# Kernel optimization log

Measured on AMD Instinct MI355X. Metric: run time of the kernel, lower is better.

The kernel has to match this reference:

```python
import jax, jax.numpy as jnp
import numpy as np

B, C_ENC, H, W = 8, 512, 96, 96
N_SAMP = 64            # num_samples in forward
N_NODES = 2 * N_SAMP   # 64 pos + 64 neg per image
D = 256                # node feature dim after head_in_ln
N_HEADS = 8
DH = D // N_HEADS
SINKHORN_ITERS = 10


def _ln(x):
    # LayerNorm(elementwise_affine=False)
    m = x.mean(-1, keepdims=True)
    v = x.var(-1, keepdims=True)
    return (x - m) / jnp.sqrt(v + 1e-5)


def setup_inputs() -> dict:
    key = jax.random.key(0)
    ks = jax.random.split(key, 12)
    std = 0.01  # matches nn.init.normal_(std=0.01) in _init_weights
    inp = {
        "feat_s": jax.random.normal(ks[0], (B, C_ENC, H, W), jnp.float32),
        "score_s": jax.random.normal(ks[1], (B, 1, H, W), jnp.float32),
        "feat_t": jax.random.normal(ks[2], (B, C_ENC, H, W), jnp.float32),
        "score_t": jax.random.normal(ks[3], (B, 1, H, W), jnp.float32),
        "head_W1": std * jax.random.normal(ks[4], (C_ENC, D), jnp.float32),
        "head_b1": jnp.zeros((D,), jnp.float32),
        "head_W2": std * jax.random.normal(ks[5], (D, D), jnp.float32),
        "head_b2": jnp.zeros((D,), jnp.float32),
        "intra_W": jax.random.normal(ks[6], (4, D, D), jnp.float32) / jnp.sqrt(jnp.float32(D)),
        "intra_b": jnp.zeros((4, D), jnp.float32),
        "cross_W": jax.random.normal(ks[7], (4, D, D), jnp.float32) / jnp.sqrt(jnp.float32(D)),
        "cross_b": jnp.zeros((4, D), jnp.float32),
        "cls_W1": std * jax.random.normal(ks[8], (D, 128), jnp.float32),
        "cls_b1": jnp.zeros((128,), jnp.float32),
        "cls_W2": std * jax.random.normal(ks[9], (128, 1), jnp.float32),
        "cls_b2": jnp.zeros((1,), jnp.float32),
        "aff_A": jax.random.normal(ks[10], (D, D), jnp.float32) / jnp.sqrt(jnp.float32(D)),
    }
    return inp


def _sample_points(feat, score):
    # torch version: boolean-mask nonzero + random gather of 64 pos / 64 neg spatial
    # locations per image. JIT-friendly deterministic equivalent: top-64 highest
    # sigmoid scores = positives, top-64 lowest = negatives.
    s = jax.nn.sigmoid(score[:, 0].reshape(B, -1))            # [B, H*W]
    _, pos_idx = jax.lax.top_k(s, N_SAMP)
    _, neg_idx = jax.lax.top_k(-s, N_SAMP)
    idx = jnp.concatenate([pos_idx, neg_idx], axis=1)         # [B, 128]
    ff = feat.reshape(B, C_ENC, -1)                           # [B, 512, H*W]
    nodes = jnp.take_along_axis(ff, idx[:, None, :], axis=2)  # [B, 512, 128]
    nodes = nodes.transpose(0, 2, 1)                          # [B, 128, 512]
    labels = jnp.concatenate(
        [jnp.ones((B, N_SAMP, 1), feat.dtype), jnp.zeros((B, N_SAMP, 1), feat.dtype)], axis=1)
    return nodes, labels


def _mha(xq, xkv, Wp, bp):
    # standard multi-head attention (MultiHeadAttentionWrapper)
    q = xq @ Wp[0] + bp[0]
    k = xkv @ Wp[1] + bp[1]
    v = xkv @ Wp[2] + bp[2]
    sh = lambda t: t.reshape(t.shape[0], t.shape[1], N_HEADS, DH)
    att = jnp.einsum("bqhd,bkhd->bhqk", sh(q), sh(k)) / jnp.sqrt(jnp.float32(DH))
    att = jax.nn.softmax(att, axis=-1)
    o = jnp.einsum("bhqk,bkhd->bqhd", att, sh(v)).reshape(xq.shape[0], xq.shape[1], D)
    return o @ Wp[3] + bp[3], att.mean(1)


def _forward(feat_s, score_s, feat_t, score_t, head_W1, head_b1, head_W2, head_b2,
             intra_W, intra_b, cross_W, cross_b, cls_W1, cls_b1, cls_W2, cls_b2, aff_A):
    n1, l1 = _sample_points(feat_s, score_s)
    n2, l2 = _sample_points(feat_t, score_t)

    # head_in_ln: Linear -> LN -> ReLU -> Linear -> LN
    head = lambda x: _ln(jax.nn.relu(_ln(x @ head_W1 + head_b1)) @ head_W2 + head_b2)
    n1, n2 = head(n1), head(n2)

    # intra-domain graph (self-attention), shared weights for both domains
    n1, _ = _mha(n1, n1, intra_W, intra_b)
    n2, _ = _mha(n2, n2, intra_W, intra_b)

    # cross-domain graph (cross-attention both directions, shared weights)
    c1, _ = _mha(n1, n2, cross_W, cross_b)
    c2, _ = _mha(n2, n1, cross_W, cross_b)
    n1, n2 = c1, c2

    # node classification loss (BCEWithLogits, mean)
    cls = lambda x: jax.nn.relu(x @ cls_W1 + cls_b1) @ cls_W2 + cls_b2
    def bce_logits(logit, lab):
        return jnp.mean(jnp.maximum(logit, 0) - logit * lab + jnp.log1p(jnp.exp(-jnp.abs(logit))))
    node_loss = bce_logits(cls(n1), l1) + bce_logits(cls(n2), l2)

    # affinity + InstanceNorm2d(1) + sinkhorn refine
    Mmat = jnp.einsum("bnd,de,bme->bnm", n1, aff_A, n2)       # [B, 128, 128]
    mu = Mmat.mean((1, 2), keepdims=True)
    var = Mmat.var((1, 2), keepdims=True)
    K = (Mmat - mu) / jnp.sqrt(var + 1e-5)
    for _ in range(SINKHORN_ITERS):  # log-space row/col normalization
        K = K - jax.nn.logsumexp(K, axis=2, keepdims=True)
        K = K - jax.nn.logsumexp(K, axis=1, keepdims=True)
    P = jnp.exp(K)

    # matching loss = BCEFocalLoss(gamma=2, alpha=0.25) vs label-agreement matrix
    gt = (l1[:, :, 0][:, :, None] == l2[:, :, 0][:, None, :]).astype(P.dtype)
    pt = jnp.clip(P, 1e-6, 1.0 - 1e-6)
    mat_loss = jnp.mean(-0.25 * (1 - pt) ** 2 * gt * jnp.log(pt)
                        - 0.75 * pt ** 2 * (1 - gt) * jnp.log(1 - pt))

    total_loss = node_loss + 10.0 * mat_loss
    return n1, total_loss


def reference(feat_s, score_s, feat_t, score_t, head_W1, head_b1, head_W2, head_b2,
              intra_W, intra_b, cross_W, cross_b, cls_W1, cls_b1, cls_W2, cls_b2, aff_A):
    return _forward(feat_s, score_s, feat_t, score_t, head_W1, head_b1, head_W2, head_b2,
                    intra_W, intra_b, cross_W, cross_b, cls_W1, cls_b1, cls_W2, cls_b2, aff_A)
```

## Files before the change

### kernel.cpp

```cpp
#include <hip/hip_runtime.h>
#include <math.h>

#define BIMG 8
#define HW 9216
#define CENC 512
#define NN 128
#define DD 256
#define NHEAD 8
#define DH 32
#define ROWS1 1024
#define ROWS2 2048
#define TAILB 520

typedef unsigned long long ull;
typedef unsigned short u16;
typedef __attribute__((ext_vector_type(4))) float f32x4;
typedef __attribute__((ext_vector_type(4))) unsigned u32x4;
typedef __attribute__((ext_vector_type(2))) unsigned u32x2;

__device__ __forceinline__ u16 f2bf(float f) {
  unsigned u = __float_as_uint(f);
  u += 0x7fffu + ((u >> 16) & 1u);
  return (u16)(u >> 16);
}
__device__ __forceinline__ float bf2f(unsigned h) { return __uint_as_float(h << 16); }
__device__ __forceinline__ unsigned pack2(float a, float b) {
  return (unsigned)f2bf(a) | ((unsigned)f2bf(b) << 16);
}
__device__ __forceinline__ void mfma_b(f32x4& acc, u32x4 a, u32x4 b) {
  asm volatile("v_mfma_f32_16x16x32_bf16 %0, %1, %2, %0" : "+v"(acc) : "v"(a), "v"(b));
}

__device__ __forceinline__ ull cmpex_keep(ull k, ull o, bool keepMax) {
  return ((k > o) == keepMax) ? k : o;
}
__device__ __forceinline__ void bsort64(ull& k, int lane) {
#pragma unroll
  for (int size = 2; size <= 64; size <<= 1) {
#pragma unroll
    for (int stride = size >> 1; stride > 0; stride >>= 1) {
      ull o = __shfl_xor(k, stride);
      bool keepMax = (((lane & size) == 0) == ((lane & stride) == 0));
      k = cmpex_keep(k, o, keepMax);
    }
  }
}
__device__ __forceinline__ void bmerge64(ull& top, ull b, int lane) {
  ull rev = __shfl_xor(b, 63);
  ull m = top > rev ? top : rev;
#pragma unroll
  for (int stride = 32; stride > 0; stride >>= 1) {
    ull o = __shfl_xor(m, stride);
    m = cmpex_keep(m, o, (lane & stride) == 0);
  }
  top = m;
}

__global__ __launch_bounds__(256) void head_kernel(const float* __restrict__ score_s,
                                                   const float* __restrict__ score_t,
                                                   int* __restrict__ idx_out,
                                                   float* __restrict__ loss_acc,
                                                   const float* __restrict__ hw1,
                                                   const float* __restrict__ hw2,
                                                   const float* __restrict__ iw,
                                                   const float* __restrict__ cw,
                                                   const float* __restrict__ aw,
                                                   const float* __restrict__ clsW1,
                                                   u16* __restrict__ wt,
                                                   u16* __restrict__ w1t) {
  __shared__ ull sm[256];
  __shared__ float tile[32][33];
  int tid = threadIdx.x;
  if (blockIdx.x < 32) {
    int blk = blockIdx.x;
    int bi = blk >> 1, neg = blk & 1;
    int lane = tid & 63, w = tid >> 6;
    if (blk == 0 && tid < 4) loss_acc[tid] = 0.f;
    const float* sp = (bi < 8 ? score_s : score_t) + (size_t)(bi & 7) * HW;
    int q0 = w * 36;
    ull keys[36];
#pragma unroll
    for (int j = 0; j < 36; ++j) {
      float x = sp[(q0 + j) * 64 + lane];
      unsigned ub = __float_as_uint(x);
      unsigned u = (ub & 0x80000000u) ? ~ub : (ub | 0x80000000u);
      if (neg) u = ~u;
      int gi = (q0 + j) * 64 + lane;
      keys[j] = ((ull)u << 32) | (unsigned)(~gi);
    }
    ull top1 = keys[0];  bsort64(top1, lane);
    ull top2 = keys[18]; bsort64(top2, lane);
#pragma unroll
    for (int j = 1; j < 18; ++j) {
      ull k1 = keys[j], k2 = keys[18 + j];
      bsort64(k1, lane);
      bsort64(k2, lane);
      bmerge64(top1, k1, lane);
      bmerge64(top2, k2, lane);
    }
    bmerge64(top1, top2, lane);
    sm[w * 64 + lane] = top1;
    __syncthreads();
    if (w < 2) {
      ull a = sm[(2 * w) * 64 + lane];
      ull b = sm[(2 * w + 1) * 64 + (63 - lane)];
      ull m = a > b ? a : b;
#pragma unroll
      for (int stride = 32; stride > 0; stride >>= 1) {
        ull o = __shfl_xor(m, stride);
        m = cmpex_keep(m, o, (lane & stride) == 0);
      }
      sm[(2 * w) * 64 + lane] = m;
    }
    __syncthreads();
    if (w == 0) {
      ull a = sm[lane];
      ull b = sm[128 + (63 - lane)];
      ull m = a > b ? a : b;
#pragma unroll
      for (int stride = 32; stride > 0; stride >>= 1) {
        ull o = __shfl_xor(m, stride);
        m = cmpex_keep(m, o, (lane & stride) == 0);
      }
      idx_out[bi * NN + neg * 64 + lane] = (int)(~(unsigned)(m & 0xffffffffull));
    }
  } else if (blockIdx.x < 800) {
    int bid = blockIdx.x - 32;
    const float* src; u16* dst; int K, k0, n0;
    if (bid < 128) {
      src = hw1; dst = wt; K = 512;
      k0 = (bid >> 3) * 32; n0 = (bid & 7) * 32;
    } else {
      int id2 = bid - 128;
      int m = id2 >> 6, tt = id2 & 63;
      K = 256;
      k0 = (tt >> 3) * 32; n0 = (tt & 7) * 32;
      src = (m == 0) ? hw2 : (m < 5) ? iw + (size_t)(m - 1) * 65536
          : (m < 9) ? cw + (size_t)(m - 5) * 65536 : aw;
      dst = wt + 131072 + (size_t)m * 65536;
    }
    int r = tid >> 3, c = (tid & 7) * 4;
    float4 v = *(const float4*)&src[(size_t)(k0 + r) * 256 + n0 + c];
    tile[r][c] = v.x; tile[r][c + 1] = v.y; tile[r][c + 2] = v.z; tile[r][c + 3] = v.w;
    __syncthreads();
    u32x2 o;
    o[0] = pack2(tile[c][r], tile[c + 1][r]);
    o[1] = pack2(tile[c + 2][r], tile[c + 3][r]);
    *(u32x2*)&dst[(size_t)(n0 + r) * K + k0 + c] = o;
  } else {
    int bid3 = blockIdx.x - 800;
    int k0 = (bid3 >> 2) * 32, n0 = (bid3 & 3) * 32;
    int r = tid >> 3, c = (tid & 7) * 4;
    float4 v = *(const float4*)&clsW1[(size_t)(k0 + r) * 128 + n0 + c];
    tile[r][c] = v.x; tile[r][c + 1] = v.y; tile[r][c + 2] = v.z; tile[r][c + 3] = v.w;
    __syncthreads();
    u32x2 o;
    o[0] = pack2(tile[c][r], tile[c + 1][r]);
    o[1] = pack2(tile[c + 2][r], tile[c + 3][r]);
    *(u32x2*)&w1t[(size_t)(n0 + r) * 256 + k0 + c] = o;
  }
}

__global__ __launch_bounds__(256) void gemm1_fused(const float* __restrict__ feat_s,
                                                   const float* __restrict__ feat_t,
                                                   const int* __restrict__ idxb,
                                                   const u16* __restrict__ wt_h1,
                                                   const float* __restrict__ head_b1,
                                                   u16* __restrict__ bufA,
                                                   float* __restrict__ st1) {
  __shared__ u16 As[16][520];
  __shared__ u16 Bs[256][40];
  int t = threadIdx.x, l = t & 63, cg = t >> 6;
  int m0 = blockIdx.x * 16;
#pragma unroll
  for (int row = 0; row < 16; ++row) {
    int grow = m0 + row;
    int bi = grow >> 7, n = grow & 127, b = bi & 7;
    const float* fp = (bi < 8) ? feat_s : feat_t;
    int pos = idxb[bi * NN + n];
    const float* src = fp + (size_t)b * CENC * HW + pos;
    float f0 = src[(size_t)(2 * t) * HW];
    float f1 = src[(size_t)(2 * t + 1) * HW];
    *(unsigned*)&As[row][2 * t] = pack2(f0, f1);
  }
  __syncthreads();
  f32x4 acc[4];
#pragma unroll
  for (int i = 0; i < 4; ++i) acc[i] = (f32x4){0.f, 0.f, 0.f, 0.f};
  for (int kc = 0; kc < 16; ++kc) {
#pragma unroll
    for (int i = 0; i < 4; ++i) {
      int e = t + i * 256;
      int nn2 = e >> 2, ch8 = (e & 3) * 8;
      *(u32x4*)&Bs[nn2][ch8] = *(const u32x4*)&wt_h1[(size_t)nn2 * 512 + kc * 32 + ch8];
    }
    __syncthreads();
    u32x4 af = *(const u32x4*)&As[l & 15][kc * 32 + (l >> 4) * 8];
#pragma unroll
    for (int i = 0; i < 4; ++i) {
      u32x4 bf = *(const u32x4*)&Bs[cg * 64 + i * 16 + (l & 15)][(l >> 4) * 8];
      mfma_b(acc[i], af, bf);
    }
    __syncthreads();
  }
  asm volatile("s_nop 7\n\ts_nop 7" ::);
  int rbase = m0 + (l >> 4) * 4;
#pragma unroll
  for (int i = 0; i < 4; ++i) {
    int col = cg * 64 + i * 16 + (l & 15);
    float bb = head_b1[col];
#pragma unroll
    for (int r = 0; r < 4; ++r) {
      int row = rbase + r;
      float o = acc[i][r] + bb;
      bufA[(size_t)row * 256 + col] = f2bf(o);
      float s = o, q = o * o;
#pragma unroll
      for (int m = 1; m < 16; m <<= 1) { s += __shfl_xor(s, m); q += __shfl_xor(q, m); }
      if ((l & 15) == 0) {
        st1[(size_t)row * 32 + cg * 4 + i]      = s;
        st1[(size_t)row * 32 + 16 + cg * 4 + i] = q;
      }
    }
  }
}

template<int K>
__global__ __launch_bounds__(256) void gemm_mf(const u16* __restrict__ A,
                                               const u16* __restrict__ Wt,
                                               const float* __restrict__ bias,
                                               u16* __restrict__ Cb,
                                               float* __restrict__ Cf,
                                               int ldc, int f32rows,
                                               const float* __restrict__ in_stats, int in_relu,
                                               float* __restrict__ out_stats,
                                               int Az, int Wz, int Cbz, int Cfz, int bz) {
  constexpr int LDK = K + 8;
  constexpr int KC = K / 8;
  __shared__ u16 As[32][LDK];
  __shared__ u16 Bs[64][LDK];
  __shared__ float mS[32], rS[32];
  int z = blockIdx.z;
  A  += (size_t)z * Az;
  Wt += (size_t)z * Wz;
  if (Cb)   Cb += (size_t)z * Cbz;
  if (Cf)   Cf += (size_t)z * Cfz;
  if (bias) bias += (size_t)z * bz;
  int n0 = blockIdx.x * 64, m0 = blockIdx.y * 32;
  int t = threadIdx.x;
  if (in_stats) {
    if (t < 32) {
      const float* sp = in_stats + (size_t)(m0 + t) * 32;
      float s = 0.f, q = 0.f;
#pragma unroll
      for (int i = 0; i < 16; ++i) { s += sp[i]; q += sp[16 + i]; }
      float mm = s * (1.f / 256.f);
      float var = q * (1.f / 256.f) - mm * mm;
      mS[t] = mm;
      rS[t] = rsqrtf(fmaxf(var, 0.f) + 1e-5f);
    }
    __syncthreads();
  }
  for (int i = t; i < 32 * KC; i += 256) {
    int row = i / KC, c8 = (i % KC) * 8;
    u32x4 av = *(const u32x4*)&A[(size_t)(m0 + row) * K + c8];
    if (in_stats) {
      float mm = mS[row], rr = rS[row];
#pragma unroll
      for (int j = 0; j < 4; ++j) {
        float f0 = (bf2f(av[j] & 0xffffu) - mm) * rr;
        float f1 = (bf2f(av[j] >> 16) - mm) * rr;
        if (in_relu) { f0 = fmaxf(f0, 0.f); f1 = fmaxf(f1, 0.f); }
        av[j] = pack2(f0, f1);
      }
    }
    *(u32x4*)&As[row][c8] = av;
  }
  for (int i = t; i < 64 * KC; i += 256) {
    int row = i / KC, c8 = (i % KC) * 8;
    *(u32x4*)&Bs[row][c8] = *(const u32x4*)&Wt[(size_t)(n0 + row) * K + c8];
  }
  __syncthreads();
  int l = t & 63, w = t >> 6;
  int wr = w >> 1, wc = w & 1;
  int fra = wr * 16 + (l & 15);
  int frk = (l >> 4) * 8;
  int fb0 = wc * 32 + (l & 15), fb1 = fb0 + 16;
  f32x4 acc0 = {0.f, 0.f, 0.f, 0.f};
  f32x4 acc1 = {0.f, 0.f, 0.f, 0.f};
#pragma unroll
  for (int ks = 0; ks < K / 32; ++ks) {
    u32x4 af = *(const u32x4*)&As[fra][ks * 32 + frk];
    u32x4 b0 = *(const u32x4*)&Bs[fb0][ks * 32 + frk];
    u32x4 b1 = *(const u32x4*)&Bs[fb1][ks * 32 + frk];
    mfma_b(acc0, af, b0);
    mfma_b(acc1, af, b1);
  }
  asm volatile("s_nop 7\n\ts_nop 7" ::);
  int col0 = n0 + wc * 32 + (l & 15);
  int rbase = m0 + wr * 16 + (l >> 4) * 4;
  float b0 = 0.f, b1 = 0.f;
  if (bias) { b0 = bias[col0]; b1 = bias[col0 + 16]; }
#pragma unroll
  for (int r = 0; r < 4; ++r) {
    int row = rbase + r;
    float o0 = acc0[r] + b0;
    float o1 = acc1[r] + b1;
    if (Cb) {
      Cb[(size_t)row * 256 + col0]      = f2bf(o0);
      Cb[(size_t)row * 256 + col0 + 16] = f2bf(o1);
    }
    if (Cf && row < ROWS1) {
      Cf[(size_t)row * ldc + col0]      = o0;
      Cf[(size_t)row * ldc + col0 + 16] = o1;
    }
    if (out_stats) {
      float s0 = o0, q0 = o0 * o0, s1 = o1, q1 = o1 * o1;
#pragma unroll
      for (int m = 1; m < 16; m <<= 1) {
        s0 += __shfl_xor(s0, m); q0 += __shfl_xor(q0, m);
        s1 += __shfl_xor(s1, m); q1 += __shfl_xor(q1, m);
      }
      if ((l & 15) == 0) {
        int base = (n0 >> 4) + wc * 2;
        out_stats[(size_t)row * 32 + base]          = s0;
        out_stats[(size_t)row * 32 + base + 1]      = s1;
        out_stats[(size_t)row * 32 + 16 + base]     = q0;
        out_stats[(size_t)row * 32 + 16 + base + 1] = q1;
      }
    }
  }
}

__global__ __launch_bounds__(256) void attn_kernel(const u16* __restrict__ q,
                                                   const u16* __restrict__ k,
                                                   const u16* __restrict__ v,
                                                   u16* __restrict__ o, int swap) {
  __shared__ __align__(16) float Ks[NN][DH];
  __shared__ __align__(16) float Vs[NN][DH];
  __shared__ __align__(16) float Ex[64][3][34];
  int blk = blockIdx.x;
  int bb = blk >> 4, h = (blk >> 1) & 7, qh = blk & 1;
  int kb = swap ? (bb ^ 8) : bb;
  int t = threadIdx.x;
  int rr = t & 63, part = t >> 6;
  for (int e = t; e < 1024; e += 256) {
    int which = e >> 9;
    int idx2 = e & 511;
    int r = idx2 >> 2, c8 = (idx2 & 3) * 8;
    u32x4 val = *(const u32x4*)&(which ? v : k)[(size_t)(kb * NN + r) * DD + h * DH + c8];
    float* dst = which ? &Vs[r][c8] : &Ks[r][c8];
#pragma unroll
    for (int i = 0; i < 4; ++i) {
      dst[2 * i]     = bf2f(val[i] & 0xffffu);
      dst[2 * i + 1] = bf2f(val[i] >> 16);
    }
  }
  __syncthreads();
  int qrow = bb * NN + qh * 64 + rr;
  float4 q4[8];
  {
    const u16* qp = q + (size_t)qrow * DD + h * DH;
#pragma unroll
    for (int c4 = 0; c4 < 4; ++c4) {
      u32x4 u = *(const u32x4*)&qp[c4 * 8];
      q4[c4 * 2].x = bf2f(u[0] & 0xffffu); q4[c4 * 2].y = bf2f(u[0] >> 16);
      q4[c4 * 2].z = bf2f(u[1] & 0xffffu); q4[c4 * 2].w = bf2f(u[1] >> 16);
      q4[c4 * 2 + 1].x = bf2f(u[2] & 0xffffu); q4[c4 * 2 + 1].y = bf2f(u[2] >> 16);
      q4[c4 * 2 + 1].z = bf2f(u[3] & 0xffffu); q4[c4 * 2 + 1].w = bf2f(u[3] >> 16);
    }
  }
  const float scale = 0.17677669529663687f;
  int j0 = part * 32;
  float mx = -1e30f;
  for (int j = j0; j < j0 + 32; ++j) {
    const float4* kp = (const float4*)Ks[j];
    float s = 0.f;
#pragma unroll
    for (int c4 = 0; c4 < 8; ++c4) {
      float4 kv = kp[c4];
      s += q4[c4].x * kv.x + q4[c4].y * kv.y + q4[c4].z * kv.z + q4[c4].w * kv.w;
    }
    mx = fmaxf(mx, s * scale);
  }
  float acc[DH];
#pragma unroll
  for (int c = 0; c < DH; ++c) acc[c] = 0.f;
  float den = 0.f;
  for (int j = j0; j < j0 + 32; ++j) {
    const float4* kp = (const float4*)Ks[j];
    float s = 0.f;
#pragma unroll
    for (int c4 = 0; c4 < 8; ++c4) {
      float4 kv = kp[c4];
      s += q4[c4].x * kv.x + q4[c4].y * kv.y + q4[c4].z * kv.z + q4[c4].w * kv.w;
    }
    float e = __expf(s * scale - mx);
    den += e;
    const float4* vp = (const float4*)Vs[j];
#pragma unroll
    for (int c4 = 0; c4 < 8; ++c4) {
      float4 vv = vp[c4];
      acc[c4 * 4 + 0] += e * vv.x; acc[c4 * 4 + 1] += e * vv.y;
      acc[c4 * 4 + 2] += e * vv.z; acc[c4 * 4 + 3] += e * vv.w;
    }
  }
  if (part) {
#pragma unroll
    for (int c = 0; c < DH; ++c) Ex[rr][part - 1][c] = acc[c];
    Ex[rr][part - 1][32] = mx;
    Ex[rr][part - 1][33] = den;
  }
  __syncthreads();
  if (part == 0) {
    float M = mx;
#pragma unroll
    for (int p = 0; p < 3; ++p) M = fmaxf(M, Ex[rr][p][32]);
    float f0 = __expf(mx - M);
    float fp[3];
    float dt = den * f0;
#pragma unroll
    for (int p = 0; p < 3; ++p) { fp[p] = __expf(Ex[rr][p][32] - M); dt += Ex[rr][p][33] * fp[p]; }
    float inv = 1.0f / dt;
    unsigned ovu[16];
#pragma unroll
    for (int c = 0; c < 16; ++c) {
      float x0 = acc[2 * c] * f0, x1 = acc[2 * c + 1] * f0;
#pragma unroll
      for (int p = 0; p < 3; ++p) { x0 += Ex[rr][p][2 * c] * fp[p]; x1 += Ex[rr][p][2 * c + 1] * fp[p]; }
      ovu[c] = pack2(x0 * inv, x1 * inv);
    }
    unsigned* op = (unsigned*)(o + (size_t)qrow * DD + h * DH);
#pragma unroll
    for (int i = 0; i < 4; ++i) {
      u32x4 w4;
      w4[0] = ovu[4 * i]; w4[1] = ovu[4 * i + 1]; w4[2] = ovu[4 * i + 2]; w4[3] = ovu[4 * i + 3];
      *(u32x4*)&op[4 * i] = w4;
    }
  }
}

struct SkSmem {
  union { u16 tmpL[128][264]; float Km[128][133]; } u;
  float u_[NN];
  float v_[NN];
  float red[20];
};
struct ClsSmem {
  float xs[4][256];
  float part[4][128];
  float red[8];
};
union TailSmem { SkSmem sk; ClsSmem cls; };

__device__ __forceinline__ void ticket_finalize(float* acc, float* out) {
  __threadfence();
  int tk = atomicAdd((int*)acc + 3, 1);
  if (tk == TAILB - 1) {
    float a0 = atomicAdd(acc + 0, 0.0f);
    float a1 = atomicAdd(acc + 1, 0.0f);
    out[ROWS1 * DD] = a0 + 10.0f * a1;
  }
}

__global__ __launch_bounds__(1024) void tail_kernel(const u16* __restrict__ bufH,
                                                    const u16* __restrict__ wt_af,
                                                    const u16* __restrict__ w1t,
                                                    const float* __restrict__ b1,
                                                    const float* __restrict__ W2,
                                                    const float* __restrict__ b2,
                                                    float* __restrict__ acc,
                                                    float* __restrict__ out) {
  __shared__ TailSmem sm;
  int t = threadIdx.x;
  int bid = blockIdx.x;
  if (bid < 8) {
    int b = bid;
    int l = t & 63, w = t >> 6;
    int tr = w >> 1;
    const u16* c1 = bufH + (size_t)(b * 128) * 256;
    const u16* c2 = bufH + (size_t)(1024 + b * 128) * 256;
    {
      int tcB = (w & 1) * 8;
      f32x4 accA[8];
#pragma unroll
      for (int i = 0; i < 8; ++i) accA[i] = (f32x4){0.f, 0.f, 0.f, 0.f};
      for (int ks = 0; ks < 8; ++ks) {
        int kk = ks * 32 + (l >> 4) * 8;
        u32x4 af = *(const u32x4*)&c1[(size_t)(tr * 16 + (l & 15)) * 256 + kk];
#pragma unroll
        for (int i = 0; i < 8; ++i) {
          u32x4 bf = *(const u32x4*)&wt_af[(size_t)((tcB + i) * 16 + (l & 15)) * 256 + kk];
          mfma_b(accA[i], af, bf);
        }
      }
      asm volatile("s_nop 7\n\ts_nop 7" ::);
      int rb = tr * 16 + (l >> 4) * 4;
#pragma unroll
      for (int i = 0; i < 8; ++i) {
        int col = (tcB + i) * 16 + (l & 15);
#pragma unroll
        for (int r2 = 0; r2 < 4; ++r2)
          sm.sk.u.tmpL[rb + r2][col] = f2bf(accA[i][r2]);
      }
    }
    __syncthreads();
    f32x4 aB[4];
    {
      int tcB = (w & 1) * 4;
#pragma unroll
      for (int i = 0; i < 4; ++i) aB[i] = (f32x4){0.f, 0.f, 0.f, 0.f};
      for (int ks = 0; ks < 8; ++ks) {
        int kk = ks * 32 + (l >> 4) * 8;
        u32x4 af = *(const u32x4*)&sm.sk.u.tmpL[tr * 16 + (l & 15)][kk];
#pragma unroll
        for (int i = 0; i < 4; ++i) {
          u32x4 bf = *(const u32x4*)&c2[(size_t)((tcB + i) * 16 + (l & 15)) * 256 + kk];
          mfma_b(aB[i], af, bf);
        }
      }
      asm volatile("s_nop 7\n\ts_nop 7" ::);
    }
    __syncthreads();
    {
      int tcB = (w & 1) * 4;
      int rb = tr * 16 + (l >> 4) * 4;
#pragma unroll
      for (int i = 0; i < 4; ++i) {
        int col = (tcB + i) * 16 + (l & 15);
#pragma unroll
        for (int r2 = 0; r2 < 4; ++r2)
          sm.sk.u.Km[rb + r2][col] = aB[i][r2];
      }
    }
    __syncthreads();
    int r = t >> 3, cg = t & 7;
    int c = t >> 3, rg = t & 7;
    float kr[16], kc[16];
    {
#pragma unroll
      for (int q4 = 0; q4 < 4; ++q4) {
        float4 f = *(const float4*)&sm.sk.u.Km[r][cg * 16 + q4 * 4];
        kr[q4 * 4 + 0] = f.x; kr[q4 * 4 + 1] = f.y; kr[q4 * 4 + 2] = f.z; kr[q4 * 4 + 3] = f.w;
      }
#pragma unroll
      for (int q = 0; q < 16; ++q)
        kc[q] = sm.sk.u.Km[rg * 16 + q][c];
    }
    float s = 0.f;
#pragma unroll
    for (int q = 0; q < 16; ++q) s += kr[q];
    for (int m = 1; m < 64; m <<= 1) s += __shfl_xor(s, m);
    if ((t & 63) == 0) sm.sk.red[t >> 6] = s;
    __syncthreads();
    if (t == 0) { float tt = 0.f; for (int i = 0; i < 16; ++i) tt += sm.sk.red[i]; sm.sk.red[16] = tt; }
    __syncthreads();
    float mu = sm.sk.red[16] * (1.0f / 16384.f);
    __syncthreads();
    float sq = 0.f;
#pragma unroll
    for (int q = 0; q < 16; ++q) { float d = kr[q] - mu; sq += d * d; }
    for (int m = 1; m < 64; m <<= 1) sq += __shfl_xor(sq, m);
    if ((t & 63) == 0) sm.sk.red[t >> 6] = sq;
    __syncthreads();
    if (t == 0) { float tt = 0.f; for (int i = 0; i < 16; ++i) tt += sm.sk.red[i]; sm.sk.red[17] = tt; }
    __syncthreads();
    float inv = 1.0f / sqrtf(sm.sk.red[17] * (1.0f / 16384.f) + 1e-5f);
#pragma unroll
    for (int q = 0; q < 16; ++q) { kr[q] = (kr[q] - mu) * inv; kc[q] = (kc[q] - mu) * inv; }
    if (t < NN) { sm.sk.u_[t] = 0.f; sm.sk.v_[t] = 0.f; }
    __syncthreads();
    for (int iter = 0; iter < 10; ++iter) {
      float tmp[16];
      {
        const float4* vp = (const float4*)(sm.sk.v_ + cg * 16);
#pragma unroll
        for (int q4 = 0; q4 < 4; ++q4) {
          float4 f = vp[q4];
          tmp[q4 * 4 + 0] = kr[q4 * 4 + 0] - f.x; tmp[q4 * 4 + 1] = kr[q4 * 4 + 1] - f.y;
          tmp[q4 * 4 + 2] = kr[q4 * 4 + 2] - f.z; tmp[q4 * 4 + 3] = kr[q4 * 4 + 3] - f.w;
        }
        float mx = tmp[0];
#pragma unroll
        for (int q = 1; q < 16; ++q) mx = fmaxf(mx, tmp[q]);
        for (int m = 1; m < 8; m <<= 1) mx = fmaxf(mx, __shfl_xor(mx, m));
        float smv = 0.f;
#pragma unroll
        for (int q = 0; q < 16; ++q) smv += __expf(tmp[q] - mx);
        for (int m = 1; m < 8; m <<= 1) smv += __shfl_xor(smv, m);
        if (cg == 0) sm.sk.u_[r] = mx + __logf(smv);
      }
      __syncthreads();
      {
        const float4* up = (const float4*)(sm.sk.u_ + rg * 16);
#pragma unroll
        for (int q4 = 0; q4 < 4; ++q4) {
          float4 f = up[q4];
          tmp[q4 * 4 + 0] = kc[q4 * 4 + 0] - f.x; tmp[q4 * 4 + 1] = kc[q4 * 4 + 1] - f.y;
          tmp[q4 * 4 + 2] = kc[q4 * 4 + 2] - f.z; tmp[q4 * 4 + 3] = kc[q4 * 4 + 3] - f.w;
        }
        float mx = tmp[0];
#pragma unroll
        for (int q = 1; q < 16; ++q) mx = fmaxf(mx, tmp[q]);
        for (int m = 1; m < 8; m <<= 1) mx = fmaxf(mx, __shfl_xor(mx, m));
        float smv = 0.f;
#pragma unroll
        for (int q = 0; q < 16; ++q) smv += __expf(tmp[q] - mx);
        for (int m = 1; m < 8; m <<= 1) smv += __shfl_xor(smv, m);
        if (rg == 0) sm.sk.v_[c] = mx + __logf(smv);
      }
      __syncthreads();
    }
    float ur = sm.sk.u_[r];
    float fsum = 0.f;
    {
      const float4* vp = (const float4*)(sm.sk.v_ + cg * 16);
#pragma unroll
      for (int q4 = 0; q4 < 4; ++q4) {
        float4 f = vp[q4];
        float vv[4] = {f.x, f.y, f.z, f.w};
#pragma unroll
        for (int j = 0; j < 4; ++j) {
          float P = __expf(kr[q4 * 4 + j] - ur - vv[j]);
          float pt = fminf(fmaxf(P, 1e-6f), 1.0f - 1e-6f);
          int col = cg * 16 + q4 * 4 + j;
          bool gt = (r < 64) == (col < 64);
          float wgt = gt ? (-0.25f * (1.f - pt) * (1.f - pt)) : (-0.75f * pt * pt);
          float lg = gt ? __logf(pt) : __logf(1.f - pt);
          fsum += wgt * lg;
        }
      }
    }
    for (int m = 1; m < 64; m <<= 1) fsum += __shfl_xor(fsum, m);
    if ((t & 63) == 0) sm.sk.red[t >> 6] = fsum;
    __syncthreads();
    if (t == 0) {
      float tt = 0.f; for (int i = 0; i < 16; ++i) tt += sm.sk.red[i];
      atomicAdd(acc + 1, tt * (1.0f / 131072.f));
      ticket_finalize(acc, out);
    }
  } else {
    int row0 = (bid - 8) * 4;
    {
      int rr = t >> 8, cc = t & 255;
      sm.cls.xs[rr][cc] = bf2f(bufH[(size_t)(row0 + rr) * 256 + cc]);
    }
    __syncthreads();
    int grp = t >> 8, col = t & 127, kh = (t >> 7) & 1;
    const u16* wp = w1t + (size_t)col * 256 + kh * 128;
    const float* xp = &sm.cls.xs[grp][kh * 128];
    float h = 0.f;
#pragma unroll
    for (int i = 0; i < 16; ++i) {
      u32x4 wv = *(const u32x4*)&wp[i * 8];
      const float* x8 = xp + i * 8;
      h += x8[0] * bf2f(wv[0] & 0xffffu) + x8[1] * bf2f(wv[0] >> 16)
         + x8[2] * bf2f(wv[1] & 0xffffu) + x8[3] * bf2f(wv[1] >> 16)
         + x8[4] * bf2f(wv[2] & 0xffffu) + x8[5] * bf2f(wv[2] >> 16)
         + x8[6] * bf2f(wv[3] & 0xffffu) + x8[7] * bf2f(wv[3] >> 16);
    }
    if (kh == 1) sm.cls.part[grp][col] = h;
    __syncthreads();
    if (kh == 0) {
      float z = h + sm.cls.part[grp][col] + b1[col];
      float p = fmaxf(z, 0.f) * W2[col];
#pragma unroll
      for (int m = 1; m < 64; m <<= 1) p += __shfl_xor(p, m);
      if ((t & 63) == 0) sm.cls.red[grp * 2 + ((t >> 6) & 1)] = p;
    }
    __syncthreads();
    if (t == 0) {
      float total = 0.f;
      float bb2 = b2[0];
#pragma unroll
      for (int g = 0; g < 4; ++g) {
        float z = sm.cls.red[2 * g] + sm.cls.red[2 * g + 1] + bb2;
        float lab = (((row0 + g) & 127) < 64) ? 1.f : 0.f;
        total += fmaxf(z, 0.f) - z * lab + log1pf(__expf(-fabsf(z)));
      }
      atomicAdd(acc, total * (1.0f / 1024.0f));
      ticket_finalize(acc, out);
    }
  }
}

extern "C" void kernel_launch(void* const* d_in, const int* in_sizes, int n_in,
                              void* d_out, int out_size, void* d_ws, size_t ws_size,
                              hipStream_t stream) {
  const float* feat_s  = (const float*)d_in[0];
  const float* score_s = (const float*)d_in[1];
  const float* feat_t  = (const float*)d_in[2];
  const float* score_t = (const float*)d_in[3];
  const float* head_W1 = (const float*)d_in[4];
  const float* head_b1 = (const float*)d_in[5];
  const float* head_W2 = (const float*)d_in[6];
  const float* head_b2 = (const float*)d_in[7];
  const float* intra_W = (const float*)d_in[8];
  const float* intra_b = (const float*)d_in[9];
  const float* cross_W = (const float*)d_in[10];
  const float* cross_b = (const float*)d_in[11];
  const float* cls_W1  = (const float*)d_in[12];
  const float* cls_b1  = (const float*)d_in[13];
  const float* cls_W2  = (const float*)d_in[14];
  const float* cls_b2  = (const float*)d_in[15];
  const float* aff_A   = (const float*)d_in[16];

  u16* bufA  = (u16*)d_ws;
  u16* bufB  = bufA + ROWS2 * DD;
  u16* bufH  = bufB + ROWS2 * DD;
  u16* qkv   = bufH + ROWS2 * DD;
  u16* attnb = qkv + 3 * ROWS2 * DD;
  u16* wt    = attnb + ROWS2 * DD;
  u16* w1t   = wt + 786432;
  float* st1 = (float*)(w1t + 32768);
  float* st2 = st1 + ROWS2 * 32;
  float* acc = st2 + ROWS2 * 32;
  int* idxb  = (int*)(acc + 8);
  float* out_f = (float*)d_out;

  u16* wt_h1 = wt;
  u16* wt_h2 = wt + 131072;
  u16* wt_in = wt_h2 + 65536;
  u16* wt_cr = wt_in + 4 * 65536;
  u16* wt_af = wt_cr + 4 * 65536;

  head_kernel<<<832, 256, 0, stream>>>(score_s, score_t, idxb, acc,
                                       head_W1, head_W2, intra_W, cross_W, aff_A, cls_W1,
                                       wt, w1t);
  gemm1_fused<<<128, 256, 0, stream>>>(feat_s, feat_t, idxb, wt_h1, head_b1, bufA, st1);

  dim3 g1(4, 64, 1);
  dim3 gq(4, 64, 3);
  const float* nulf = nullptr;
  float* nulw = nullptr;

  gemm_mf<256><<<g1, 256, 0, stream>>>(bufA, wt_h2, head_b2, bufB, nulw,
                                       0, 0, st1, 1, st2, 0, 0, 0, 0, 0);
  gemm_mf<256><<<gq, 256, 0, stream>>>(bufB, wt_in, intra_b, qkv, nulw,
                                       0, 0, st2, 0, nulw, 0, 65536, ROWS2 * DD, 0, 256);
  attn_kernel<<<256, 256, 0, stream>>>(qkv, qkv + ROWS2 * DD, qkv + 2 * ROWS2 * DD,
                                       attnb, 0);
  gemm_mf<256><<<g1, 256, 0, stream>>>(attnb, wt_in + 3 * 65536, intra_b + 768, bufH, nulw,
                                       0, 0, nulf, 0, nulw, 0, 0, 0, 0, 0);
  gemm_mf<256><<<gq, 256, 0, stream>>>(bufH, wt_cr, cross_b, qkv, nulw,
                                       0, 0, nulf, 0, nulw, 0, 65536, ROWS2 * DD, 0, 256);
  attn_kernel<<<256, 256, 0, stream>>>(qkv, qkv + ROWS2 * DD, qkv + 2 * ROWS2 * DD,
                                       attnb, 1);
  gemm_mf<256><<<g1, 256, 0, stream>>>(attnb, wt_cr + 3 * 65536, cross_b + 768, bufH, out_f,
                                       256, 0, nulf, 0, nulw, 0, 0, 0, 0, 0);
  tail_kernel<<<TAILB, 1024, 0, stream>>>(bufH, wt_af, w1t, cls_b1, cls_W2, cls_b2,
                                          acc, out_f);
}
```

Measured before the change: 216.8 us.

## Fold intra output projection into cross QKV weights and fuse QKV GEMMs

The intra-attention output projection is algebraically folded into the cross-attention Q/K/V weights (Wo·Wc and bias bo·Wc + bc), precomputed in extra head_kernel blocks. This removes one full GEMM launch between the two attention stages. A new gemm_qkv kernel loads the A tile once and loops over the three Q/K/V weight sets, replacing the z-batched grid. In exchange, the folded weight product adds fp32 matmul work in the setup kernel and rounds the combined weight to bf16 once, which changes numerics slightly.

```diff
diff --git a/kernel.cpp b/kernel.cpp
--- a/kernel.cpp
+++ b/kernel.cpp
@@ -66,10 +66,16 @@
                                                    const float* __restrict__ cw,
                                                    const float* __restrict__ aw,
                                                    const float* __restrict__ clsW1,
+                                                   const float* __restrict__ intra_b,
+                                                   const float* __restrict__ cross_b,
                                                    u16* __restrict__ wt,
-                                                   u16* __restrict__ w1t) {
-  __shared__ ull sm[256];
-  __shared__ float tile[32][33];
+                                                   u16* __restrict__ w1t,
+                                                   u16* __restrict__ wt_f,
+                                                   float* __restrict__ bfq) {
+  __shared__ union {
+    struct { ull sm[256]; float tile[32][33]; } a;
+    struct { float Wo[32][264]; float Wc[256][40]; } b;
+  } HS;
   int tid = threadIdx.x;
   if (blockIdx.x < 32) {
     int blk = blockIdx.x;
@@ -99,23 +105,23 @@
       bmerge64(top2, k2, lane);
     }
     bmerge64(top1, top2, lane);
-    sm[w * 64 + lane] = top1;
+    HS.a.sm[w * 64 + lane] = top1;
     __syncthreads();
     if (w < 2) {
-      ull a = sm[(2 * w) * 64 + lane];
-      ull b = sm[(2 * w + 1) * 64 + (63 - lane)];
+      ull a = HS.a.sm[(2 * w) * 64 + lane];
+      ull b = HS.a.sm[(2 * w + 1) * 64 + (63 - lane)];
       ull m = a > b ? a : b;
 #pragma unroll
       for (int stride = 32; stride > 0; stride >>= 1) {
         ull o = __shfl_xor(m, stride);
         m = cmpex_keep(m, o, (lane & stride) == 0);
       }
-      sm[(2 * w) * 64 + lane] = m;
+      HS.a.sm[(2 * w) * 64 + lane] = m;
     }
     __syncthreads();
     if (w == 0) {
-      ull a = sm[lane];
-      ull b = sm[128 + (63 - lane)];
+      ull a = HS.a.sm[lane];
+      ull b = HS.a.sm[128 + (63 - lane)];
       ull m = a > b ? a : b;
 #pragma unroll
       for (int stride = 32; stride > 0; stride >>= 1) {
@@ -141,23 +147,61 @@
     }
     int r = tid >> 3, c = (tid & 7) * 4;
     float4 v = *(const float4*)&src[(size_t)(k0 + r) * 256 + n0 + c];
-    tile[r][c] = v.x; tile[r][c + 1] = v.y; tile[r][c + 2] = v.z; tile[r][c + 3] = v.w;
+    HS.a.tile[r][c] = v.x; HS.a.tile[r][c + 1] = v.y;
+    HS.a.tile[r][c + 2] = v.z; HS.a.tile[r][c + 3] = v.w;
     __syncthreads();
     u32x2 o;
-    o[0] = pack2(tile[c][r], tile[c + 1][r]);
-    o[1] = pack2(tile[c + 2][r], tile[c + 3][r]);
+    o[0] = pack2(HS.a.tile[c][r], HS.a.tile[c + 1][r]);
+    o[1] = pack2(HS.a.tile[c + 2][r], HS.a.tile[c + 3][r]);
     *(u32x2*)&dst[(size_t)(n0 + r) * K + k0 + c] = o;
-  } else {
+  } else if (blockIdx.x < 832) {
     int bid3 = blockIdx.x - 800;
     int k0 = (bid3 >> 2) * 32, n0 = (bid3 & 3) * 32;
     int r = tid >> 3, c = (tid & 7) * 4;
     float4 v = *(const float4*)&clsW1[(size_t)(k0 + r) * 128 + n0 + c];
-    tile[r][c] = v.x; tile[r][c + 1] = v.y; tile[r][c + 2] = v.z; tile[r][c + 3] = v.w;
+    HS.a.tile[r][c] = v.x; HS.a.tile[r][c + 1] = v.y;
+    HS.a.tile[r][c + 2] = v.z; HS.a.tile[r][c + 3] = v.w;
     __syncthreads();
     u32x2 o;
-    o[0] = pack2(tile[c][r], tile[c + 1][r]);
-    o[1] = pack2(tile[c + 2][r], tile[c + 3][r]);
+    o[0] = pack2(HS.a.tile[c][r], HS.a.tile[c + 1][r]);
+    o[1] = pack2(HS.a.tile[c + 2][r], HS.a.tile[c + 3][r]);
     *(u32x2*)&w1t[(size_t)(n0 + r) * 256 + k0 + c] = o;
+  } else {
+    int bid4 = blockIdx.x - 832;
+    int z = bid4 >> 6, tt = bid4 & 63;
+    int k0 = (tt >> 3) * 32, n0 = (tt & 7) * 32;
+    const float* Wo = iw + 3 * 65536;
+    const float* Wc = cw + (size_t)z * 65536;
+    for (int e = tid; e < 2048; e += 256) {
+      int row = e >> 6, c4 = (e & 63) * 4;
+      float4 v = *(const float4*)&Wo[(size_t)(k0 + row) * 256 + c4];
+      *(float4*)&HS.b.Wo[row][c4] = v;
+    }
+    for (int e = tid; e < 2048; e += 256) {
+      int row = e >> 3, c4 = (e & 7) * 4;
+      float4 v = *(const float4*)&Wc[(size_t)row * 256 + n0 + c4];
+      *(float4*)&HS.b.Wc[row][c4] = v;
+    }
+    __syncthreads();
+    int k = tid >> 3, nb = (tid & 7) * 4;
+    float a0 = 0.f, a1 = 0.f, a2 = 0.f, a3 = 0.f;
+#pragma unroll 8
+    for (int j = 0; j < 256; ++j) {
+      float wo = HS.b.Wo[k][j];
+      float4 wc = *(const float4*)&HS.b.Wc[j][nb];
+      a0 += wo * wc.x; a1 += wo * wc.y; a2 += wo * wc.z; a3 += wo * wc.w;
+    }
+    u16* dst = wt_f + (size_t)z * 65536;
+    dst[(size_t)(n0 + nb + 0) * 256 + k0 + k] = f2bf(a0);
+    dst[(size_t)(n0 + nb + 1) * 256 + k0 + k] = f2bf(a1);
+    dst[(size_t)(n0 + nb + 2) * 256 + k0 + k] = f2bf(a2);
+    dst[(size_t)(n0 + nb + 3) * 256 + k0 + k] = f2bf(a3);
+    if (k0 == 0 && tid < 32) {
+      float b = 0.f;
+      const float* bo = intra_b + 768;
+      for (int j = 0; j < 256; ++j) b += bo[j] * HS.b.Wc[j][tid];
+      bfq[z * 256 + n0 + tid] = b + cross_b[z * 256 + n0 + tid];
+    }
   }
 }
 
@@ -231,21 +275,14 @@
                                                const float* __restrict__ bias,
                                                u16* __restrict__ Cb,
                                                float* __restrict__ Cf,
-                                               int ldc, int f32rows,
+                                               int ldc,
                                                const float* __restrict__ in_stats, int in_relu,
-                                               float* __restrict__ out_stats,
-                                               int Az, int Wz, int Cbz, int Cfz, int bz) {
+                                               float* __restrict__ out_stats) {
   constexpr int LDK = K + 8;
   constexpr int KC = K / 8;
   __shared__ u16 As[32][LDK];
   __shared__ u16 Bs[64][LDK];
   __shared__ float mS[32], rS[32];
-  int z = blockIdx.z;
-  A  += (size_t)z * Az;
-  Wt += (size_t)z * Wz;
-  if (Cb)   Cb += (size_t)z * Cbz;
-  if (Cf)   Cf += (size_t)z * Cfz;
-  if (bias) bias += (size_t)z * bz;
   int n0 = blockIdx.x * 64, m0 = blockIdx.y * 32;
   int t = threadIdx.x;
   if (in_stats) {
@@ -328,6 +365,81 @@
         out_stats[(size_t)row * 32 + 16 + base]     = q0;
         out_stats[(size_t)row * 32 + 16 + base + 1] = q1;
       }
+    }
+  }
+}
+
+template<int HASLN>
+__global__ __launch_bounds__(256) void gemm_qkv(const u16* __restrict__ A,
+                                                const u16* __restrict__ Wt,
+                                                const float* __restrict__ bias,
+                                                u16* __restrict__ C,
+                                                const float* __restrict__ in_stats) {
+  __shared__ u16 As[32][264];
+  __shared__ u16 Bs[64][264];
+  __shared__ float mS[32], rS[32];
+  int n0 = blockIdx.x * 64, m0 = blockIdx.y * 32;
+  int t = threadIdx.x;
+  if (HASLN) {
+    if (t < 32) {
+      const float* sp = in_stats + (size_t)(m0 + t) * 32;
+      float s = 0.f, q = 0.f;
+#pragma unroll
+      for (int i = 0; i < 16; ++i) { s += sp[i]; q += sp[16 + i]; }
+      float mm = s * (1.f / 256.f);
+      mS[t] = mm;
+      rS[t] = rsqrtf(fmaxf(q * (1.f / 256.f) - mm * mm, 0.f) + 1e-5f);
+    }
+    __syncthreads();
+  }
+  for (int i = t; i < 32 * 32; i += 256) {
+    int row = i >> 5, c8 = (i & 31) * 8;
+    u32x4 av = *(const u32x4*)&A[(size_t)(m0 + row) * 256 + c8];
+    if (HASLN) {
+      float mm = mS[row], rr = rS[row];
+#pragma unroll
+      for (int j = 0; j < 4; ++j) {
+        float f0 = (bf2f(av[j] & 0xffffu) - mm) * rr;
+        float f1 = (bf2f(av[j] >> 16) - mm) * rr;
+        av[j] = pack2(f0, f1);
+      }
+    }
+    *(u32x4*)&As[row][c8] = av;
+  }
+  int l = t & 63, w = t >> 6;
+  int wr = w >> 1, wc = w & 1;
+  int fra = wr * 16 + (l & 15);
+  int frk = (l >> 4) * 8;
+  int fb0 = wc * 32 + (l & 15), fb1 = fb0 + 16;
+  int col0 = n0 + wc * 32 + (l & 15);
+  int rbase = m0 + wr * 16 + (l >> 4) * 4;
+#pragma unroll
+  for (int z = 0; z < 3; ++z) {
+    __syncthreads();
+    for (int i = t; i < 64 * 32; i += 256) {
+      int row = i >> 5, c8 = (i & 31) * 8;
+      *(u32x4*)&Bs[row][c8] =
+          *(const u32x4*)&Wt[(size_t)z * 65536 + (size_t)(n0 + row) * 256 + c8];
+    }
+    __syncthreads();
+    f32x4 acc0 = {0.f, 0.f, 0.f, 0.f};
+    f32x4 acc1 = {0.f, 0.f, 0.f, 0.f};
+#pragma unroll
+    for (int ks = 0; ks < 8; ++ks) {
+      u32x4 af = *(const u32x4*)&As[fra][ks * 32 + frk];
+      u32x4 b0 = *(const u32x4*)&Bs[fb0][ks * 32 + frk];
+      u32x4 b1 = *(const u32x4*)&Bs[fb1][ks * 32 + frk];
+      mfma_b(acc0, af, b0);
+      mfma_b(acc1, af, b1);
+    }
+    asm volatile("s_nop 7\n\ts_nop 7" ::);
+    float b0 = bias[z * 256 + col0], b1 = bias[z * 256 + col0 + 16];
+    u16* Cz = C + (size_t)z * ROWS2 * DD;
+#pragma unroll
+    for (int r = 0; r < 4; ++r) {
+      int row = rbase + r;
+      Cz[(size_t)row * 256 + col0]      = f2bf(acc0[r] + b0);
+      Cz[(size_t)row * 256 + col0 + 16] = f2bf(acc1[r] + b1);
     }
   }
 }
@@ -712,9 +824,11 @@
   u16* attnb = qkv + 3 * ROWS2 * DD;
   u16* wt    = attnb + ROWS2 * DD;
   u16* w1t   = wt + 786432;
-  float* st1 = (float*)(w1t + 32768);
+  u16* wt_f  = w1t + 32768;
+  float* st1 = (float*)(wt_f + 3 * 65536);
   float* st2 = st1 + ROWS2 * 32;
-  float* acc = st2 + ROWS2 * 32;
+  float* bfq = st2 + ROWS2 * 32;
+  float* acc = bfq + 768;
   int* idxb  = (int*)(acc + 8);
   float* out_f = (float*)d_out;
 
@@ -724,30 +838,25 @@
   u16* wt_cr = wt_in + 4 * 65536;
   u16* wt_af = wt_cr + 4 * 65536;
 
-  head_kernel<<<832, 256, 0, stream>>>(score_s, score_t, idxb, acc,
-                                       head_W1, head_W2, intra_W, cross_W, aff_A, cls_W1,
-                                       wt, w1t);
+  head_kernel<<<1024, 256, 0, stream>>>(score_s, score_t, idxb, acc,
+                                        head_W1, head_W2, intra_W, cross_W, aff_A, cls_W1,
+                                        intra_b, cross_b, wt, w1t, wt_f, bfq);
   gemm1_fused<<<128, 256, 0, stream>>>(feat_s, feat_t, idxb, wt_h1, head_b1, bufA, st1);
 
   dim3 g1(4, 64, 1);
-  dim3 gq(4, 64, 3);
   const float* nulf = nullptr;
   float* nulw = nullptr;
-
-  gemm_mf<256><<<g1, 256, 0, stream>>>(bufA, wt_h2, head_b2, bufB, nulw,
-                                       0, 0, st1, 1, st2, 0, 0, 0, 0, 0);
-  gemm_mf<256><<<gq, 256, 0, stream>>>(bufB, wt_in, intra_b, qkv, nulw,
-                                       0, 0, st2, 0, nulw, 0, 65536, ROWS2 * DD, 0, 256);
+  u16* nulb = nullptr;
+
+  gemm_mf<256><<<g1, 256, 0, stream>>>(bufA, wt_h2, head_b2, bufB, nulw, 0, st1, 1, st2);
+  gemm_qkv<1><<<g1, 256, 0, stream>>>(bufB, wt_in, intra_b, qkv, st2);
   attn_kernel<<<256, 256, 0, stream>>>(qkv, qkv + ROWS2 * DD, qkv + 2 * ROWS2 * DD,
                                        attnb, 0);
-  gemm_mf<256><<<g1, 256, 0, stream>>>(attnb, wt_in + 3 * 65536, intra_b + 768, bufH, nulw,
-                                       0, 0, nulf, 0, nulw, 0, 0, 0, 0, 0);
-  gemm_mf<256><<<gq, 256, 0, stream>>>(bufH, wt_cr, cross_b, qkv, nulw,
-                                       0, 0, nulf, 0, nulw, 0, 65536, ROWS2 * DD, 0, 256);
+  gemm_qkv<0><<<g1, 256, 0, stream>>>(attnb, wt_f, bfq, qkv, nulf);
   attn_kernel<<<256, 256, 0, stream>>>(qkv, qkv + ROWS2 * DD, qkv + 2 * ROWS2 * DD,
                                        attnb, 1);
   gemm_mf<256><<<g1, 256, 0, stream>>>(attnb, wt_cr + 3 * 65536, cross_b + 768, bufH, out_f,
-                                       256, 0, nulf, 0, nulw, 0, 0, 0, 0, 0);
+                                       256, nulf, 0, nulw);
   tail_kernel<<<TAILB, 1024, 0, stream>>>(bufH, wt_af, w1t, cls_b1, cls_W2, cls_b2,
                                           acc, out_f);
 }
```

After: 221.3 us. 1.02x slower.

## Fold intra-attention output projection into cross-attention QKV weights

Applied to the files above, without the earlier changes.

Precomputes the product of the intra-attention output projection and the three cross-attention Q/K/V weights, plus the folded bias, inside the head kernel. This removes one GEMM launch and its intermediate buffer from the chain. The head kernel also moves to 512 threads, so the top-k sort runs across 8 waves with shorter per-wave key lists. The fused weights are rounded to bf16 after the fp32 product, which changes rounding slightly and adds a small weight-fusion GEMM to the head kernel.

```diff
diff --git a/kernel.cpp b/kernel.cpp
--- a/kernel.cpp
+++ b/kernel.cpp
@@ -55,8 +55,17 @@
   }
   top = m;
 }
-
-__global__ __launch_bounds__(256) void head_kernel(const float* __restrict__ score_s,
+__device__ __forceinline__ ull lds_merge(ull a, ull brev, int lane) {
+  ull m = a > brev ? a : brev;
+#pragma unroll
+  for (int stride = 32; stride > 0; stride >>= 1) {
+    ull o = __shfl_xor(m, stride);
+    m = cmpex_keep(m, o, (lane & stride) == 0);
+  }
+  return m;
+}
+
+__global__ __launch_bounds__(512) void head_kernel(const float* __restrict__ score_s,
                                                    const float* __restrict__ score_t,
                                                    int* __restrict__ idx_out,
                                                    float* __restrict__ loss_acc,
@@ -66,10 +75,16 @@
                                                    const float* __restrict__ cw,
                                                    const float* __restrict__ aw,
                                                    const float* __restrict__ clsW1,
+                                                   const float* __restrict__ intra_b,
+                                                   const float* __restrict__ cross_b,
                                                    u16* __restrict__ wt,
-                                                   u16* __restrict__ w1t) {
-  __shared__ ull sm[256];
-  __shared__ float tile[32][33];
+                                                   u16* __restrict__ w1t,
+                                                   u16* __restrict__ wt_f,
+                                                   float* __restrict__ bfq) {
+  __shared__ union {
+    struct { ull sm[512]; float tile[32][33]; } a;
+    struct { float Wo[32][264]; float Wc[256][40]; } b;
+  } HS;
   int tid = threadIdx.x;
   if (blockIdx.x < 32) {
     int blk = blockIdx.x;
@@ -77,10 +92,10 @@
     int lane = tid & 63, w = tid >> 6;
     if (blk == 0 && tid < 4) loss_acc[tid] = 0.f;
     const float* sp = (bi < 8 ? score_s : score_t) + (size_t)(bi & 7) * HW;
-    int q0 = w * 36;
-    ull keys[36];
-#pragma unroll
-    for (int j = 0; j < 36; ++j) {
+    int q0 = w * 18;
+    ull keys[18];
+#pragma unroll
+    for (int j = 0; j < 18; ++j) {
       float x = sp[(q0 + j) * 64 + lane];
       unsigned ub = __float_as_uint(x);
       unsigned u = (ub & 0x80000000u) ? ~ub : (ub | 0x80000000u);
@@ -88,40 +103,33 @@
       int gi = (q0 + j) * 64 + lane;
       keys[j] = ((ull)u << 32) | (unsigned)(~gi);
     }
-    ull top1 = keys[0];  bsort64(top1, lane);
-    ull top2 = keys[18]; bsort64(top2, lane);
-#pragma unroll
-    for (int j = 1; j < 18; ++j) {
-      ull k1 = keys[j], k2 = keys[18 + j];
+    ull top1 = keys[0]; bsort64(top1, lane);
+    ull top2 = keys[9]; bsort64(top2, lane);
+#pragma unroll
+    for (int j = 1; j < 9; ++j) {
+      ull k1 = keys[j], k2 = keys[9 + j];
       bsort64(k1, lane);
       bsort64(k2, lane);
       bmerge64(top1, k1, lane);
       bmerge64(top2, k2, lane);
     }
     bmerge64(top1, top2, lane);
-    sm[w * 64 + lane] = top1;
+    HS.a.sm[w * 64 + lane] = top1;
+    __syncthreads();
+    if (w < 4) {
+      ull m = lds_merge(HS.a.sm[(2 * w) * 64 + lane],
+                        HS.a.sm[(2 * w + 1) * 64 + (63 - lane)], lane);
+      HS.a.sm[(2 * w) * 64 + lane] = m;
+    }
     __syncthreads();
     if (w < 2) {
-      ull a = sm[(2 * w) * 64 + lane];
-      ull b = sm[(2 * w + 1) * 64 + (63 - lane)];
-      ull m = a > b ? a : b;
-#pragma unroll
-      for (int stride = 32; stride > 0; stride >>= 1) {
-        ull o = __shfl_xor(m, stride);
-        m = cmpex_keep(m, o, (lane & stride) == 0);
-      }
-      sm[(2 * w) * 64 + lane] = m;
+      ull m = lds_merge(HS.a.sm[(4 * w) * 64 + lane],
+                        HS.a.sm[(4 * w + 2) * 64 + (63 - lane)], lane);
+      HS.a.sm[(4 * w) * 64 + lane] = m;
     }
     __syncthreads();
     if (w == 0) {
-      ull a = sm[lane];
-      ull b = sm[128 + (63 - lane)];
-      ull m = a > b ? a : b;
-#pragma unroll
-      for (int stride = 32; stride > 0; stride >>= 1) {
-        ull o = __shfl_xor(m, stride);
-        m = cmpex_keep(m, o, (lane & stride) == 0);
-      }
+      ull m = lds_merge(HS.a.sm[lane], HS.a.sm[4 * 64 + (63 - lane)], lane);
       idx_out[bi * NN + neg * 64 + lane] = (int)(~(unsigned)(m & 0xffffffffull));
     }
   } else if (blockIdx.x < 800) {
@@ -140,24 +148,73 @@
       dst = wt + 131072 + (size_t)m * 65536;
     }
     int r = tid >> 3, c = (tid & 7) * 4;
-    float4 v = *(const float4*)&src[(size_t)(k0 + r) * 256 + n0 + c];
-    tile[r][c] = v.x; tile[r][c + 1] = v.y; tile[r][c + 2] = v.z; tile[r][c + 3] = v.w;
-    __syncthreads();
-    u32x2 o;
-    o[0] = pack2(tile[c][r], tile[c + 1][r]);
-    o[1] = pack2(tile[c + 2][r], tile[c + 3][r]);
-    *(u32x2*)&dst[(size_t)(n0 + r) * K + k0 + c] = o;
-  } else {
+    if (tid < 256) {
+      float4 v = *(const float4*)&src[(size_t)(k0 + r) * 256 + n0 + c];
+      HS.a.tile[r][c] = v.x; HS.a.tile[r][c + 1] = v.y;
+      HS.a.tile[r][c + 2] = v.z; HS.a.tile[r][c + 3] = v.w;
+    }
+    __syncthreads();
+    if (tid < 256) {
+      u32x2 o;
+      o[0] = pack2(HS.a.tile[c][r], HS.a.tile[c + 1][r]);
+      o[1] = pack2(HS.a.tile[c + 2][r], HS.a.tile[c + 3][r]);
+      *(u32x2*)&dst[(size_t)(n0 + r) * K + k0 + c] = o;
+    }
+  } else if (blockIdx.x < 832) {
     int bid3 = blockIdx.x - 800;
     int k0 = (bid3 >> 2) * 32, n0 = (bid3 & 3) * 32;
     int r = tid >> 3, c = (tid & 7) * 4;
-    float4 v = *(const float4*)&clsW1[(size_t)(k0 + r) * 128 + n0 + c];
-    tile[r][c] = v.x; tile[r][c + 1] = v.y; tile[r][c + 2] = v.z; tile[r][c + 3] = v.w;
-    __syncthreads();
-    u32x2 o;
-    o[0] = pack2(tile[c][r], tile[c + 1][r]);
-    o[1] = pack2(tile[c + 2][r], tile[c + 3][r]);
-    *(u32x2*)&w1t[(size_t)(n0 + r) * 256 + k0 + c] = o;
+    if (tid < 256) {
+      float4 v = *(const float4*)&clsW1[(size_t)(k0 + r) * 128 + n0 + c];
+      HS.a.tile[r][c] = v.x; HS.a.tile[r][c + 1] = v.y;
+      HS.a.tile[r][c + 2] = v.z; HS.a.tile[r][c + 3] = v.w;
+    }
+    __syncthreads();
+    if (tid < 256) {
+      u32x2 o;
+      o[0] = pack2(HS.a.tile[c][r], HS.a.tile[c + 1][r]);
+      o[1] = pack2(HS.a.tile[c + 2][r], HS.a.tile[c + 3][r]);
+      *(u32x2*)&w1t[(size_t)(n0 + r) * 256 + k0 + c] = o;
+    }
+  } else {
+    int bid4 = blockIdx.x - 832;
+    int z = bid4 >> 6, tt = bid4 & 63;
+    int k0 = (tt >> 3) * 32, n0 = (tt & 7) * 32;
+    const float* Wo = iw + 3 * 65536;
+    const float* Wc = cw + (size_t)z * 65536;
+    for (int e = tid; e < 2048; e += 512) {
+      int row = e >> 6, c4 = (e & 63) * 4;
+      *(float4*)&HS.b.Wo[row][c4] = *(const float4*)&Wo[(size_t)(k0 + row) * 256 + c4];
+    }
+    for (int e = tid; e < 2048; e += 512) {
+      int row = e >> 3, c4 = (e & 7) * 4;
+      *(float4*)&HS.b.Wc[row][c4] = *(const float4*)&Wc[(size_t)row * 256 + n0 + c4];
+    }
+    __syncthreads();
+    int k = tid >> 4, half = (tid >> 3) & 1, nb = (tid & 7) * 4;
+    float a0 = 0.f, a1 = 0.f, a2 = 0.f, a3 = 0.f;
+    int jb = half * 128;
+#pragma unroll 8
+    for (int j = 0; j < 128; ++j) {
+      float wo = HS.b.Wo[k][jb + j];
+      float4 wc = *(const float4*)&HS.b.Wc[jb + j][nb];
+      a0 += wo * wc.x; a1 += wo * wc.y; a2 += wo * wc.z; a3 += wo * wc.w;
+    }
+    a0 += __shfl_xor(a0, 8); a1 += __shfl_xor(a1, 8);
+    a2 += __shfl_xor(a2, 8); a3 += __shfl_xor(a3, 8);
+    if (half == 0) {
+      u16* dst = wt_f + (size_t)z * 65536;
+      dst[(size_t)(n0 + nb + 0) * 256 + k0 + k] = f2bf(a0);
+      dst[(size_t)(n0 + nb + 1) * 256 + k0 + k] = f2bf(a1);
+      dst[(size_t)(n0 + nb + 2) * 256 + k0 + k] = f2bf(a2);
+      dst[(size_t)(n0 + nb + 3) * 256 + k0 + k] = f2bf(a3);
+    }
+    if (k0 == 0 && tid < 32) {
+      float b = 0.f;
+      const float* bo = intra_b + 768;
+      for (int j = 0; j < 256; ++j) b += bo[j] * HS.b.Wc[j][tid];
+      bfq[z * 256 + n0 + tid] = b + cross_b[z * 256 + n0 + tid];
+    }
   }
 }
 
@@ -231,20 +288,18 @@
                                                const float* __restrict__ bias,
                                                u16* __restrict__ Cb,
                                                float* __restrict__ Cf,
-                                               int ldc, int f32rows,
+                                               int ldc,
                                                const float* __restrict__ in_stats, int in_relu,
                                                float* __restrict__ out_stats,
-                                               int Az, int Wz, int Cbz, int Cfz, int bz) {
+                                               int Wz, int Cbz, int bz) {
   constexpr int LDK = K + 8;
   constexpr int KC = K / 8;
   __shared__ u16 As[32][LDK];
   __shared__ u16 Bs[64][LDK];
   __shared__ float mS[32], rS[32];
   int z = blockIdx.z;
-  A  += (size_t)z * Az;
   Wt += (size_t)z * Wz;
   if (Cb)   Cb += (size_t)z * Cbz;
-  if (Cf)   Cf += (size_t)z * Cfz;
   if (bias) bias += (size_t)z * bz;
   int n0 = blockIdx.x * 64, m0 = blockIdx.y * 32;
   int t = threadIdx.x;
@@ -712,9 +767,11 @@
   u16* attnb = qkv + 3 * ROWS2 * DD;
   u16* wt    = attnb + ROWS2 * DD;
   u16* w1t   = wt + 786432;
-  float* st1 = (float*)(w1t + 32768);
+  u16* wt_f  = w1t + 32768;
+  float* st1 = (float*)(wt_f + 3 * 65536);
   float* st2 = st1 + ROWS2 * 32;
-  float* acc = st2 + ROWS2 * 32;
+  float* bfq = st2 + ROWS2 * 32;
+  float* acc = bfq + 768;
   int* idxb  = (int*)(acc + 8);
   float* out_f = (float*)d_out;
 
@@ -724,9 +781,9 @@
   u16* wt_cr = wt_in + 4 * 65536;
   u16* wt_af = wt_cr + 4 * 65536;
 
-  head_kernel<<<832, 256, 0, stream>>>(score_s, score_t, idxb, acc,
-                                       head_W1, head_W2, intra_W, cross_W, aff_A, cls_W1,
-                                       wt, w1t);
+  head_kernel<<<1024, 512, 0, stream>>>(score_s, score_t, idxb, acc,
+                                        head_W1, head_W2, intra_W, cross_W, aff_A, cls_W1,
+                                        intra_b, cross_b, wt, w1t, wt_f, bfq);
   gemm1_fused<<<128, 256, 0, stream>>>(feat_s, feat_t, idxb, wt_h1, head_b1, bufA, st1);
 
   dim3 g1(4, 64, 1);
@@ -734,20 +791,18 @@
   const float* nulf = nullptr;
   float* nulw = nullptr;
 
-  gemm_mf<256><<<g1, 256, 0, stream>>>(bufA, wt_h2, head_b2, bufB, nulw,
-                                       0, 0, st1, 1, st2, 0, 0, 0, 0, 0);
-  gemm_mf<256><<<gq, 256, 0, stream>>>(bufB, wt_in, intra_b, qkv, nulw,
-                                       0, 0, st2, 0, nulw, 0, 65536, ROWS2 * DD, 0, 256);
+  gemm_mf<256><<<g1, 256, 0, stream>>>(bufA, wt_h2, head_b2, bufB, nulw, 0, st1, 1, st2,
+                                       0, 0, 0);
+  gemm_mf<256><<<gq, 256, 0, stream>>>(bufB, wt_in, intra_b, qkv, nulw, 0, st2, 0, nulw,
+                                       65536, ROWS2 * DD, 256);
   attn_kernel<<<256, 256, 0, stream>>>(qkv, qkv + ROWS2 * DD, qkv + 2 * ROWS2 * DD,
                                        attnb, 0);
-  gemm_mf<256><<<g1, 256, 0, stream>>>(attnb, wt_in + 3 * 65536, intra_b + 768, bufH, nulw,
-                                       0, 0, nulf, 0, nulw, 0, 0, 0, 0, 0);
-  gemm_mf<256><<<gq, 256, 0, stream>>>(bufH, wt_cr, cross_b, qkv, nulw,
-                                       0, 0, nulf, 0, nulw, 0, 65536, ROWS2 * DD, 0, 256);
+  gemm_mf<256><<<gq, 256, 0, stream>>>(attnb, wt_f, bfq, qkv, nulw, 0, nulf, 0, nulw,
+                                       65536, ROWS2 * DD, 256);
   attn_kernel<<<256, 256, 0, stream>>>(qkv, qkv + ROWS2 * DD, qkv + 2 * ROWS2 * DD,
                                        attnb, 1);
   gemm_mf<256><<<g1, 256, 0, stream>>>(attnb, wt_cr + 3 * 65536, cross_b + 768, bufH, out_f,
-                                       256, 0, nulf, 0, nulw, 0, 0, 0, 0, 0);
+                                       256, nulf, 0, nulw, 0, 0, 0);
   tail_kernel<<<TAILB, 1024, 0, stream>>>(bufH, wt_af, w1t, cls_b1, cls_W2, cls_b2,
                                           acc, out_f);
 }
```

Measured after the change: 212.7 us. Within noise of the previous version (-1.9%).
